# Optimization experiments

Measured on AMD Instinct MI355X. Metric: run time of the kernel, lower is better.

The kernel has to match this reference:

```python
import jax, jax.numpy as jnp
import numpy as np

B, L, LE = 2, 1024, 1024
NM, DM, NL = 80, 512, 8
LAYERS = NL // 2
DS, EXP, K, H = 16, 2, 4, 4
DI = EXP * DM            # 1024
DTR = (DM + 15) // 16    # dt_rank 'auto' -> 32
HD = DM // H             # 128


def setup_inputs() -> dict:
    key = jax.random.key(0)
    ks = iter(jax.random.split(key, 48))
    n = lambda shape, s=0.02: jax.random.normal(next(ks), shape, jnp.float32) * s
    return {
        "x": jax.random.normal(next(ks), (B, L, NM), jnp.float32),
        "enc_output": jax.random.normal(next(ks), (B, LE, DM), jnp.float32),
        "W_in": n((DM, NM)), "b_in": jnp.zeros((DM,), jnp.float32),
        "m_norm_w": jnp.ones((LAYERS, DM), jnp.float32),
        "m_in_w": n((LAYERS, 2 * DI, DM)),
        "m_conv_w": n((LAYERS, DI, K), 0.1),
        "m_conv_b": jnp.zeros((LAYERS, DI), jnp.float32),
        "m_xproj_w": n((LAYERS, DTR + 2 * DS, DI)),
        "m_dt_w": n((LAYERS, DI, DTR)),
        "m_dt_b": n((LAYERS, DI), 0.1),
        "m_Alog": jnp.tile(jnp.log(jnp.arange(1, DS + 1, dtype=jnp.float32))[None, None, :], (LAYERS, DI, 1)),
        "m_D": jnp.ones((LAYERS, DI), jnp.float32),
        "m_out_w": n((LAYERS, DM, DI)),
        "a_in_w": n((LAYERS, 3 * DM, DM)),
        "a_in_b": jnp.zeros((LAYERS, 3 * DM), jnp.float32),
        "a_out_w": n((LAYERS, DM, DM)),
        "a_out_b": jnp.zeros((LAYERS, DM), jnp.float32),
        "a_ln_w": jnp.ones((LAYERS, DM), jnp.float32),
        "a_ln_b": jnp.zeros((LAYERS, DM), jnp.float32),
        "normf_w": jnp.ones((DM,), jnp.float32),
        "W_out": n((NM, DM)),
    }


def rmsnorm(x, w, eps=1e-5):
    return x * jax.lax.rsqrt(jnp.mean(x * x, axis=-1, keepdims=True) + eps) * w


def layernorm(x, w, b, eps=1e-5):
    m = jnp.mean(x, axis=-1, keepdims=True)
    v = jnp.mean((x - m) ** 2, axis=-1, keepdims=True)
    return (x - m) * jax.lax.rsqrt(v + eps) * w + b


def dwconv_causal(x, w, b):
    # x: (B,L,DI), w: (DI,K) depthwise; torch Conv1d(padding=K-1)[..., :L] == left-pad K-1
    xt = jnp.transpose(x, (0, 2, 1))  # (B,DI,L)
    y = jax.lax.conv_general_dilated(xt, w[:, None, :], (1,), [(K - 1, 0)],
                                     feature_group_count=DI,
                                     dimension_numbers=("NCH", "OIH", "NCH"))
    return jnp.transpose(y, (0, 2, 1)) + b


def selective_scan_cumsum(u, delta, A, Bm, Cm, Dv):
    # mamba-tiny 'cumsum' scan. u,delta: (B,L,DI); A: (DI,DS); Bm,Cm: (B,L,DS); Dv: (DI,)
    dA = jnp.einsum("bld,dn->bldn", delta, A)
    dBu = jnp.einsum("bld,bld,bln->bldn", delta, u, Bm)
    shifted = jnp.pad(dA[:, 1:], ((0, 0), (0, 1), (0, 0), (0, 0)))
    dA_cs = jnp.exp(jnp.flip(jnp.cumsum(jnp.flip(shifted, 1), 1), 1))  # suffix-sum exp
    xs = jnp.cumsum(dBu * dA_cs, axis=1) / (dA_cs + 1e-12)
    y = jnp.einsum("bldn,bln->bld", xs, Cm)
    return y + u * Dv


def mamba_block(u, in_w, conv_w, conv_b, xproj_w, dt_w, dt_b, Alog, Dv, out_w):
    xr = u @ in_w.T                       # (B,L,2*DI)
    xm, res = xr[..., :DI], xr[..., DI:]
    xm = jax.nn.silu(dwconv_causal(xm, conv_w, conv_b))
    x_dbl = xm @ xproj_w.T                # (B,L,DTR+2*DS)
    dlt = x_dbl[..., :DTR]
    Bm = x_dbl[..., DTR:DTR + DS]
    Cm = x_dbl[..., DTR + DS:]
    delta = jax.nn.softplus(dlt @ dt_w.T + dt_b)
    A = -jnp.exp(Alog)
    y = selective_scan_cumsum(xm, delta, A, Bm, Cm, Dv)
    y = y * jax.nn.silu(res)
    return y @ out_w.T


def cross_attn_block(q_in, kv, in_w, in_b, out_w, out_b, ln_w, ln_b):
    Wq, Wk, Wv = in_w[:DM], in_w[DM:2 * DM], in_w[2 * DM:]
    bq, bk, bv = in_b[:DM], in_b[DM:2 * DM], in_b[2 * DM:]
    q = (q_in @ Wq.T + bq).reshape(B, -1, H, HD)
    k = (kv @ Wk.T + bk).reshape(B, -1, H, HD)
    v = (kv @ Wv.T + bv).reshape(B, -1, H, HD)
    scores = jnp.einsum("bqhd,bkhd->bhqk", q, k) / jnp.sqrt(jnp.float32(HD))
    attn = jax.nn.softmax(scores, axis=-1)
    o = jnp.einsum("bhqk,bkhd->bqhd", attn, v).reshape(B, -1, DM)
    o = o @ out_w.T + out_b
    return layernorm(q_in + o, ln_w, ln_b)  # dropout is identity in eval


def reference(x, enc_output, W_in, b_in, m_norm_w, m_in_w, m_conv_w, m_conv_b,
              m_xproj_w, m_dt_w, m_dt_b, m_Alog, m_D, m_out_w,
              a_in_w, a_in_b, a_out_w, a_out_b, a_ln_w, a_ln_b, normf_w, W_out):
    h = x @ W_in.T + b_in
    for i in range(LAYERS):
        h = h + mamba_block(rmsnorm(h, m_norm_w[i]), m_in_w[i], m_conv_w[i],
                            m_conv_b[i], m_xproj_w[i], m_dt_w[i], m_dt_b[i],
                            m_Alog[i], m_D[i], m_out_w[i])
        h = cross_attn_block(h, enc_output, a_in_w[i], a_in_b[i],
                             a_out_w[i], a_out_b[i], a_ln_w[i], a_ln_b[i])
    h = rmsnorm(h, normf_w)
    return h @ W_out.T
```

## Files before the change

### kernel.cpp

```cpp
#include <hip/hip_runtime.h>
#include <hip/hip_bf16.h>
#include <math.h>

typedef __hip_bfloat16 bf16;
typedef __attribute__((ext_vector_type(8))) short short8x;
typedef __attribute__((ext_vector_type(4))) float f32x4;

static constexpr int cB   = 2;
static constexpr int cL   = 1024;
static constexpr int cLE  = 1024;
static constexpr int cNM  = 80;
static constexpr int cDM  = 512;
static constexpr int cLAYERS = 4;
static constexpr int cDS  = 16;
static constexpr int cKC  = 4;
static constexpr int cH   = 4;
static constexpr int cDI  = 1024;
static constexpr int cDTR = 32;
static constexpr int cHD  = 128;

static constexpr int cNCH = 64;
static constexpr int cCHL = cL / cNCH;

#define GLL16(g, l) __builtin_amdgcn_global_load_lds( \
    (const __attribute__((address_space(1))) void*)(g), \
    (__attribute__((address_space(3))) void*)(l), 16, 0, 0)

template<int ACT, int BM, int BN>
__global__ __launch_bounds__(256)
void bgemm_kernel(const bf16* __restrict__ A, const bf16* __restrict__ W,
                  const float* __restrict__ bias, const float* __restrict__ addv,
                  float* __restrict__ Cf, bf16* __restrict__ Cb,
                  int M, int N, int Kd, int lda, int ldw, int ldcf, int ldcb, int ldadd,
                  int bdiv, long sA1, long sA2, long sW1, long sW2,
                  long sCf1, long sCf2, long sCb1, long sCb2, long sBias)
{
    constexpr int RM = BM / 32;
    constexpr int RN = BN / 32;
    const int z = blockIdx.z;
    const int i1 = z / bdiv, i2 = z % bdiv;
    A += i1 * sA1 + i2 * sA2;
    W += i1 * sW1 + i2 * sW2;
    if (bias) bias += i1 * sBias;

    const int bm = blockIdx.y * BM;
    const int bn = blockIdx.x * BN;
    const int tid = threadIdx.x;
    const int lane = tid & 63;
    const int wid = tid >> 6;
    const int wr = wid >> 1, wc = wid & 1;

    __shared__ bf16 As[BM * 32];
    __shared__ bf16 Bs[BN * 32];

    f32x4 acc[RM][RN] = {};

    const int r_in = lane >> 2;
    const int kb   = (lane & 3) * 8;
    const int hi   = lane >> 4;
    const int rc   = lane & 15;

    for (int k0 = 0; k0 < Kd; k0 += 32) {
#pragma unroll
        for (int iss = 0; iss < BM / 64; iss++) {
            const int row = wid * (BM / 4) + iss * 16 + r_in;
            int gm = bm + row; if (gm >= M) gm = M - 1;
            const bf16* ga = A + (long)gm * lda + k0 + kb;
            GLL16(ga, As + (wid * (BM / 4) + iss * 16) * 32);
        }
#pragma unroll
        for (int iss = 0; iss < BN / 64; iss++) {
            const int row = wid * (BN / 4) + iss * 16 + r_in;
            int gn = bn + row; if (gn >= N) gn = N - 1;
            const bf16* gb = W + (long)gn * ldw + k0 + kb;
            GLL16(gb, Bs + (wid * (BN / 4) + iss * 16) * 32);
        }
        asm volatile("s_waitcnt vmcnt(0)" ::: "memory");
        __syncthreads();

        short8x af[RM], bfv[RN];
#pragma unroll
        for (int i = 0; i < RM; i++)
            af[i] = *(const short8x*)(As + (wr * (BM / 2) + i * 16 + rc) * 32 + hi * 8);
#pragma unroll
        for (int j = 0; j < RN; j++)
            bfv[j] = *(const short8x*)(Bs + (wc * (BN / 2) + j * 16 + rc) * 32 + hi * 8);
#pragma unroll
        for (int i = 0; i < RM; i++)
#pragma unroll
            for (int j = 0; j < RN; j++)
                acc[i][j] = __builtin_amdgcn_mfma_f32_16x16x32_bf16(af[i], bfv[j], acc[i][j], 0, 0, 0);
        __syncthreads();
    }

    const long cfo = i1 * sCf1 + i2 * sCf2;
    const long cbo = i1 * sCb1 + i2 * sCb2;
#pragma unroll
    for (int i = 0; i < RM; i++) {
#pragma unroll
        for (int r = 0; r < 4; r++) {
            const int gm = bm + wr * (BM / 2) + i * 16 + hi * 4 + r;
            if (gm >= M) continue;
#pragma unroll
            for (int j = 0; j < RN; j++) {
                const int gn = bn + wc * (BN / 2) + j * 16 + rc;
                if (gn >= N) continue;
                float v = acc[i][j][r];
                if (bias) v += bias[gn];
                if (ACT == 1) v = (v > 20.f) ? v : log1pf(__expf(v));
                if (addv) v += addv[cfo + (long)gm * ldadd + gn];
                if (Cf) Cf[cfo + (long)gm * ldcf + gn] = v;
                if (Cb) Cb[cbo + (long)gm * ldcb + gn] = __float2bfloat16(v);
            }
        }
    }
}

static inline void bgemm(int ACT, int BM, int BN, const bf16* A, const bf16* W, const float* bias,
                         const float* addv, float* Cf, bf16* Cb,
                         int M, int N, int Kd, int lda, int ldw, int ldcf, int ldcb, int ldadd,
                         int nz, int bdiv, long sA1, long sA2, long sW1, long sW2,
                         long sCf1, long sCf2, long sCb1, long sCb2, long sBias, hipStream_t s)
{
    dim3 g((N + BN - 1) / BN, (M + BM - 1) / BM, nz), b(256);
#define BG_ARGS A, W, bias, addv, Cf, Cb, M, N, Kd, lda, ldw, ldcf, ldcb, ldadd, \
                bdiv, sA1, sA2, sW1, sW2, sCf1, sCf2, sCb1, sCb2, sBias
    if (BM == 128) {
        if (ACT == 1) bgemm_kernel<1, 128, 128><<<g, b, 0, s>>>(BG_ARGS);
        else          bgemm_kernel<0, 128, 128><<<g, b, 0, s>>>(BG_ARGS);
    } else if (BN == 128) {
        if (ACT == 1) bgemm_kernel<1, 64, 128><<<g, b, 0, s>>>(BG_ARGS);
        else          bgemm_kernel<0, 64, 128><<<g, b, 0, s>>>(BG_ARGS);
    } else {
        bgemm_kernel<0, 64, 64><<<g, b, 0, s>>>(BG_ARGS);
    }
#undef BG_ARGS
}

static inline void bgemm_plain(int ACT, int BM, int BN, const bf16* A, const bf16* W,
                               const float* bias, const float* addv, float* Cf, bf16* Cb,
                               int M, int N, int Kd, int lda, int ldw, int ldcf, int ldcb,
                               int ldadd, hipStream_t s)
{
    bgemm(ACT, BM, BN, A, W, bias, addv, Cf, Cb, M, N, Kd, lda, ldw, ldcf, ldcb, ldadd,
          1, 1, 0, 0, 0, 0, 0, 0, 0, 0, 0, s);
}

__global__ __launch_bounds__(128)
void flash_attn_kernel(const bf16* __restrict__ Hb, const bf16* __restrict__ Wq,
                       const float* __restrict__ bq,
                       const bf16* __restrict__ Kp, const bf16* __restrict__ VTp,
                       bf16* __restrict__ Op, float scale)
{
    const int qt = blockIdx.x;
    const int bh = blockIdx.y;
    const int b = bh >> 2, h = bh & 3;
    const int tid = threadIdx.x;
    const int w = tid >> 6;
    const int lane = tid & 63;
    const int rc = lane & 15, hi = lane >> 4;
    const int rlo = rc & 7;
    const int r_in = lane >> 2;
    const int kb   = (lane & 3) * 8;

    __shared__ bf16 Qs[32 * 128];
    __shared__ bf16 Ks[64 * 128];
    __shared__ bf16 Vs[128 * 64];
    __shared__ bf16 Ps[32 * 64];

    {
        bf16* HsT = Vs;
        bf16* WsT = Ks;
        const bf16* hb0 = Hb + ((long)(b * cL + qt * 32)) * cDM;
        const bf16* wq0 = Wq + (long)h * cHD * cDM;
        f32x4 qacc[8] = {};
        for (int k0 = 0; k0 < cDM; k0 += 32) {
            __syncthreads();
            GLL16(hb0 + (long)(w * 16 + r_in) * cDM + k0 + kb, HsT + (w * 16) * 32);
#pragma unroll
            for (int iss = 0; iss < 4; iss++)
                GLL16(wq0 + (long)(iss * 32 + w * 16 + r_in) * cDM + k0 + kb,
                      WsT + (iss * 32 + w * 16) * 32);
            asm volatile("s_waitcnt vmcnt(0)" ::: "memory");
            __syncthreads();
            short8x aH = *(const short8x*)(HsT + (w * 16 + rc) * 32 + hi * 8);
#pragma unroll
            for (int j = 0; j < 8; j++) {
                short8x bW = *(const short8x*)(WsT + (j * 16 + rc) * 32 + hi * 8);
                qacc[j] = __builtin_amdgcn_mfma_f32_16x16x32_bf16(aH, bW, qacc[j], 0, 0, 0);
            }
        }
        __syncthreads();
#pragma unroll
        for (int j2 = 0; j2 < 8; j2++)
#pragma unroll
            for (int r = 0; r < 4; r++) {
                const int qrow = w * 16 + hi * 4 + r;
                const int col = j2 * 16 + rc;
                const float qv = qacc[j2][r] + bq[h * cHD + col];
                Qs[qrow * 128 + (((col >> 3) ^ (qrow & 7)) << 3) + (col & 7)] =
                    __float2bfloat16(qv);
            }
    }
    __syncthreads();

    short8x aq[4];
#pragma unroll
    for (int kk = 0; kk < 4; kk++) {
        const int sc = (kk * 4 + hi) ^ rlo;
        aq[kk] = *(const short8x*)(Qs + (w * 16 + rc) * 128 + sc * 8);
    }

    float m_r[4], l_r[4];
#pragma unroll
    for (int r = 0; r < 4; r++) { m_r[r] = -1e30f; l_r[r] = 0.f; }
    f32x4 oacc[8] = {};

    const bf16* kb0 = Kp + ((long)(b * cLE)) * (2 * cDM) + h * cHD;
    const bf16* vb0 = VTp + ((long)(b * cDM + h * cHD)) * cLE;

    for (int kt = 0; kt < 16; kt++) {
        __syncthreads();
#pragma unroll
        for (int c = 0; c < 8; c++) {
            const int row = w * 32 + c * 4 + (lane >> 4);
            const int gc = (lane & 15) ^ (row & 7);
            GLL16(kb0 + ((long)(kt * 64 + row)) * (2 * cDM) + gc * 8,
                  Ks + (w * 32 + c * 4) * 128);
        }
#pragma unroll
        for (int c = 0; c < 8; c++) {
            const int row = w * 64 + c * 8 + (lane >> 3);
            const int gc = (lane & 7) ^ (row & 7);
            GLL16(vb0 + (long)row * cLE + kt * 64 + gc * 8,
                  Vs + (w * 64 + c * 8) * 64);
        }
        asm volatile("s_waitcnt vmcnt(0)" ::: "memory");
        __syncthreads();

        f32x4 s[4] = {};
#pragma unroll
        for (int kk = 0; kk < 4; kk++) {
            const int sc = (kk * 4 + hi) ^ rlo;
#pragma unroll
            for (int j = 0; j < 4; j++) {
                short8x bk = *(const short8x*)(Ks + (j * 16 + rc) * 128 + sc * 8);
                s[j] = __builtin_amdgcn_mfma_f32_16x16x32_bf16(aq[kk], bk, s[j], 0, 0, 0);
            }
        }

        float p[4][4];
        float esc[4];
#pragma unroll
        for (int r = 0; r < 4; r++) {
            const float v0 = s[0][r] * scale, v1 = s[1][r] * scale;
            const float v2 = s[2][r] * scale, v3 = s[3][r] * scale;
            float mx = fmaxf(fmaxf(v0, v1), fmaxf(v2, v3));
            mx = fmaxf(mx, __shfl_xor(mx, 1));
            mx = fmaxf(mx, __shfl_xor(mx, 2));
            mx = fmaxf(mx, __shfl_xor(mx, 4));
            mx = fmaxf(mx, __shfl_xor(mx, 8));
            const float mn = fmaxf(m_r[r], mx);
            p[0][r] = __expf(v0 - mn);
            p[1][r] = __expf(v1 - mn);
            p[2][r] = __expf(v2 - mn);
            p[3][r] = __expf(v3 - mn);
            float rs = (p[0][r] + p[1][r]) + (p[2][r] + p[3][r]);
            rs += __shfl_xor(rs, 1);
            rs += __shfl_xor(rs, 2);
            rs += __shfl_xor(rs, 4);
            rs += __shfl_xor(rs, 8);
            esc[r] = __expf(m_r[r] - mn);
            l_r[r] = l_r[r] * esc[r] + rs;
            m_r[r] = mn;
        }
#pragma unroll
        for (int j2 = 0; j2 < 8; j2++)
#pragma unroll
            for (int r = 0; r < 4; r++)
                oacc[j2][r] *= esc[r];
#pragma unroll
        for (int j = 0; j < 4; j++)
#pragma unroll
            for (int r = 0; r < 4; r++) {
                const int q = w * 16 + hi * 4 + r;
                const int cp = (j * 2 + (rc >> 3)) ^ (q & 7);
                Ps[q * 64 + cp * 8 + (rc & 7)] = __float2bfloat16(p[j][r]);
            }
        __syncthreads();
#pragma unroll
        for (int ks = 0; ks < 2; ks++) {
            const int sc = (ks * 4 + hi) ^ rlo;
            short8x ap = *(const short8x*)(Ps + (w * 16 + rc) * 64 + sc * 8);
#pragma unroll
            for (int j2 = 0; j2 < 8; j2++) {
                short8x bv = *(const short8x*)(Vs + (j2 * 16 + rc) * 64 + sc * 8);
                oacc[j2] = __builtin_amdgcn_mfma_f32_16x16x32_bf16(ap, bv, oacc[j2], 0, 0, 0);
            }
        }
    }

    float inv[4];
#pragma unroll
    for (int r = 0; r < 4; r++) inv[r] = 1.f / l_r[r];
    bf16* ob = Op + ((long)(b * cL + qt * 32)) * cDM + h * cHD;
#pragma unroll
    for (int j2 = 0; j2 < 8; j2++)
#pragma unroll
        for (int r = 0; r < 4; r++)
            ob[(long)(w * 16 + hi * 4 + r) * cDM + j2 * 16 + rc] =
                __float2bfloat16(oacc[j2][r] * inv[r]);
}

__global__ void splitk_reduce_kernel(const float* __restrict__ parts, float* __restrict__ outf,
                                     bf16* __restrict__ outb, int n4, int sliceN4, int S)
{
    const int i = blockIdx.x * 256 + threadIdx.x;
    if (i >= n4) return;
    float4 a = ((const float4*)parts)[i];
    for (int s2 = 1; s2 < S; s2++) {
        float4 b2 = ((const float4*)parts)[i + (long)s2 * sliceN4];
        a.x += b2.x; a.y += b2.y; a.z += b2.z; a.w += b2.w;
    }
    ((float4*)outf)[i] = a;
    bf16 b0 = __float2bfloat16(a.x), b1 = __float2bfloat16(a.y);
    bf16 b2 = __float2bfloat16(a.z), b3 = __float2bfloat16(a.w);
    short4 pk = { *(short*)&b0, *(short*)&b1, *(short*)&b2, *(short*)&b3 };
    ((short4*)outb)[i] = pk;
}

__global__ void cvt_all_kernel(
    const float* __restrict__ s0, bf16* __restrict__ d0,
    const float* __restrict__ s1, bf16* __restrict__ d1,
    const float* __restrict__ s2, bf16* __restrict__ d2,
    const float* __restrict__ s3, bf16* __restrict__ d3,
    const float* __restrict__ s4, bf16* __restrict__ d4,
    const float* __restrict__ s5, bf16* __restrict__ d5,
    const float* __restrict__ s6, bf16* __restrict__ d6,
    const float* __restrict__ s7, bf16* __restrict__ d7)
{
    constexpr long E0 = 1048576, E1 = 4194304, E2 = 262144, E3 = 131072;
    constexpr long E4 = 2097152, E5 = 3145728, E6 = 1048576, E7 = 40960;
    constexpr long C0 = E0, C1 = C0 + E1, C2 = C1 + E2, C3 = C2 + E3;
    constexpr long C4 = C3 + E4, C5 = C4 + E5, C6 = C5 + E6, C7 = C6 + E7;
    long i = ((long)blockIdx.x * 256 + threadIdx.x) * 4;
    if (i >= C7) return;
    const float* s; bf16* d;
    if      (i < C0) { s = s0; d = d0; }
    else if (i < C1) { s = s1; d = d1; i -= C0; }
    else if (i < C2) { s = s2; d = d2; i -= C1; }
    else if (i < C3) { s = s3; d = d3; i -= C2; }
    else if (i < C4) { s = s4; d = d4; i -= C3; }
    else if (i < C5) { s = s5; d = d5; i -= C4; }
    else if (i < C6) { s = s6; d = d6; i -= C5; }
    else             { s = s7; d = d7; i -= C6; }
    float4 v = *(const float4*)(s + i);
    d[i]     = __float2bfloat16(v.x);
    d[i + 1] = __float2bfloat16(v.y);
    d[i + 2] = __float2bfloat16(v.z);
    d[i + 3] = __float2bfloat16(v.w);
}

__global__ void cvt_pad_kernel(const float* __restrict__ in, bf16* __restrict__ out,
                               int rows, int kin, int kout)
{
    const int idx = blockIdx.x * 256 + threadIdx.x;
    if (idx >= rows * kout) return;
    const int r = idx / kout, k = idx - r * kout;
    out[idx] = __float2bfloat16(k < kin ? in[(long)r * kin + k] : 0.f);
}

__global__ void transpose_bf16_kernel(const bf16* __restrict__ in, bf16* __restrict__ out,
                                      int ldin, int col0, long inLS, long outLS)
{
    __shared__ bf16 t[32][33];
    const int z = blockIdx.z;
    const int lay = z >> 1, b = z & 1;
    in  += (long)lay * inLS;
    out += (long)lay * outLS;
    const int le0 = blockIdx.x * 32, d0 = blockIdx.y * 32;
    const int tid = threadIdx.x;
    const int c = tid & 31, r = tid >> 5;
    for (int i = r; i < 32; i += 8)
        t[i][c] = in[((long)b * cLE + le0 + i) * ldin + col0 + d0 + c];
    __syncthreads();
    for (int i = r; i < 32; i += 8)
        out[((long)b * cDM + d0 + i) * cLE + le0 + c] = t[c][i];
}

__global__ void rmsnorm_kernel(const float* __restrict__ x, const float* __restrict__ w,
                               float* __restrict__ outf, bf16* __restrict__ outb, int Dm)
{
    const int row = blockIdx.x;
    const float* xr = x + (long)row * Dm;
    float s = 0.f;
    for (int i = threadIdx.x; i < Dm; i += 256) { float v = xr[i]; s += v * v; }
    __shared__ float red[5];
    const int lane = threadIdx.x & 63, wv = threadIdx.x >> 6;
#pragma unroll
    for (int off = 1; off < 64; off <<= 1) s += __shfl_xor(s, off);
    if (lane == 0) red[wv] = s;
    __syncthreads();
    if (threadIdx.x == 0) {
        float t = red[0] + red[1] + red[2] + red[3];
        red[4] = rsqrtf(t / Dm + 1e-5f);
    }
    __syncthreads();
    const float scale = red[4];
    for (int i = threadIdx.x; i < Dm; i += 256) {
        float v = xr[i] * scale * w[i];
        if (outf) outf[(long)row * Dm + i] = v;
        if (outb) outb[(long)row * Dm + i] = __float2bfloat16(v);
    }
}

__global__ void layernorm_kernel(const float* __restrict__ x, const float* __restrict__ w,
                                 const float* __restrict__ b, float* __restrict__ outf,
                                 bf16* __restrict__ outb,
                                 const float* __restrict__ rms_w, bf16* __restrict__ rms_out)
{
    const int row = blockIdx.x;
    const float* xr = x + (long)row * 512;
    const int t = threadIdx.x;
    const int i0 = t, i1 = t + 256;
    float x0 = xr[i0], x1 = xr[i1];
    float s = x0 + x1, sq = x0 * x0 + x1 * x1;
    __shared__ float red[8];
    __shared__ float mv[2];
    const int lane = t & 63, wv = t >> 6;
#pragma unroll
    for (int off = 1; off < 64; off <<= 1) { s += __shfl_xor(s, off); sq += __shfl_xor(sq, off); }
    if (lane == 0) { red[wv] = s; red[4 + wv] = sq; }
    __syncthreads();
    if (t == 0) {
        float ts = red[0] + red[1] + red[2] + red[3];
        float tq = red[4] + red[5] + red[6] + red[7];
        float m = ts / 512.f;
        float var = tq / 512.f - m * m;
        mv[0] = m;
        mv[1] = rsqrtf(var + 1e-5f);
    }
    __syncthreads();
    const float m = mv[0], rs = mv[1];
    const float v0 = (x0 - m) * rs * w[i0] + b[i0];
    const float v1 = (x1 - m) * rs * w[i1] + b[i1];
    outf[(long)row * 512 + i0] = v0;
    outf[(long)row * 512 + i1] = v1;
    outb[(long)row * 512 + i0] = __float2bfloat16(v0);
    outb[(long)row * 512 + i1] = __float2bfloat16(v1);
    float s2 = v0 * v0 + v1 * v1;
#pragma unroll
    for (int off = 1; off < 64; off <<= 1) s2 += __shfl_xor(s2, off);
    if (lane == 0) red[wv] = s2;
    __syncthreads();
    if (t == 0) mv[0] = rsqrtf((red[0] + red[1] + red[2] + red[3]) / 512.f + 1e-5f);
    __syncthreads();
    const float rsc = mv[0];
    rms_out[(long)row * 512 + i0] = __float2bfloat16(v0 * rsc * rms_w[i0]);
    rms_out[(long)row * 512 + i1] = __float2bfloat16(v1 * rsc * rms_w[i1]);
}

__global__ void conv_silu_kernel(const float* __restrict__ xr, const float* __restrict__ w,
                                 const float* __restrict__ bias, float* __restrict__ xm,
                                 bf16* __restrict__ xmb)
{
    const int idx = blockIdx.x * 256 + threadIdx.x;
    if (idx >= cB * cL * cDI) return;
    const int d = idx & (cDI - 1);
    const int l = (idx >> 10) & (cL - 1);
    const int b = idx >> 20;
    float s = bias[d];
#pragma unroll
    for (int j = 0; j < cKC; j++) {
        const int ls = l + j - (cKC - 1);
        if (ls >= 0) s += w[d * cKC + j] * xr[((long)(b * cL + ls)) * (2 * cDI) + d];
    }
    s = s / (1.f + __expf(-s));
    xm[(long)idx] = s;
    xmb[(long)idx] = __float2bfloat16(s);
}

__global__ void scan_phase1(const float* __restrict__ xm, const float* __restrict__ delta,
                            const float* __restrict__ xdbl, const float* __restrict__ Alog,
                            float* __restrict__ aprod_out, float* __restrict__ send_out)
{
    const int idx4 = blockIdx.x * 256 + threadIdx.x;
    const int ng = idx4 & 3;
    const int d  = (idx4 >> 2) & (cDI - 1);
    const int ch = (idx4 >> 12) & (cNCH - 1);
    const int b  = idx4 >> 18;
    const float4 Al = *(const float4*)(Alog + d * cDS + 4 * ng);
    const float A0 = -__expf(Al.x), A1 = -__expf(Al.y), A2 = -__expf(Al.z), A3 = -__expf(Al.w);
    float s0 = 0.f, s1 = 0.f, s2 = 0.f, s3 = 0.f;
    float p0 = 1.f, p1 = 1.f, p2 = 1.f, p3 = 1.f;
    const int l0 = ch * cCHL;
    const float* dp = delta + (long)(b * cL + l0) * cDI + d;
    const float* up = xm    + (long)(b * cL + l0) * cDI + d;
    const float* xb = xdbl  + (long)(b * cL + l0) * 64 + cDTR + 4 * ng;
#pragma unroll
    for (int t = 0; t < cCHL; t++) {
        const float dl = dp[(long)t * cDI];
        const float du = dl * up[(long)t * cDI];
        const float4 Bv = *(const float4*)(xb + (long)t * 64);
        const float a0 = __expf(dl * A0), a1 = __expf(dl * A1);
        const float a2 = __expf(dl * A2), a3 = __expf(dl * A3);
        s0 = a0 * s0 + du * Bv.x; p0 *= a0;
        s1 = a1 * s1 + du * Bv.y; p1 *= a1;
        s2 = a2 * s2 + du * Bv.z; p2 *= a2;
        s3 = a3 * s3 + du * Bv.w; p3 *= a3;
    }
    const long base4 = (((long)(b * cNCH + ch) * cDI + d) * cDS) + 4 * ng;
    float4 pv = { p0, p1, p2, p3 };
    float4 sv = { s0, s1, s2, s3 };
    *(float4*)(aprod_out + base4) = pv;
    *(float4*)(send_out + base4)  = sv;
}

__global__ void scan_phase2(const float* __restrict__ aprod, const float* __restrict__ send,
                            float* __restrict__ sinit)
{
    const int j = blockIdx.x * 64 + threadIdx.x;
    const int n = j & (cDS - 1);
    const int d = (j >> 4) & (cDI - 1);
    const int b = j >> 14;
    float s = 0.f;
#pragma unroll
    for (int c = 0; c < cNCH; c++) {
        const long off = (((long)(b * cNCH + c) * cDI + d) * cDS) + n;
        sinit[off] = s;
        s = aprod[off] * s + send[off];
    }
}

__global__ void scan_phase3(const float* __restrict__ xm, const float* __restrict__ delta,
                            const float* __restrict__ xdbl, const float* __restrict__ Alog,
                            const float* __restrict__ Dv, const float* __restrict__ xr,
                            const float* __restrict__ sinit, bf16* __restrict__ y)
{
    const int idx4 = blockIdx.x * 256 + threadIdx.x;
    const int ng = idx4 & 3;
    const int d  = (idx4 >> 2) & (cDI - 1);
    const int ch = (idx4 >> 12) & (cNCH - 1);
    const int b  = idx4 >> 18;
    const float4 Al = *(const float4*)(Alog + d * cDS + 4 * ng);
    const float A0 = -__expf(Al.x), A1 = -__expf(Al.y), A2 = -__expf(Al.z), A3 = -__expf(Al.w);
    const float Dval = Dv[d];
    const long base4 = (((long)(b * cNCH + ch) * cDI + d) * cDS) + 4 * ng;
    float4 st = *(const float4*)(sinit + base4);
    float s0 = st.x, s1 = st.y, s2 = st.z, s3 = st.w;
    const int l0 = ch * cCHL;
    const float* dp = delta + (long)(b * cL + l0) * cDI + d;
    const float* up = xm    + (long)(b * cL + l0) * cDI + d;
    const float* xb = xdbl  + (long)(b * cL + l0) * 64 + cDTR + 4 * ng;
    const float* xc = xb + cDS;
    const float* rp = xr + (long)(b * cL + l0) * (2 * cDI) + cDI + d;
    bf16* yp = y + (long)(b * cL + l0) * cDI + d;
#pragma unroll
    for (int t = 0; t < cCHL; t++) {
        const float dl = dp[(long)t * cDI];
        const float u  = up[(long)t * cDI];
        const float du = dl * u;
        const float4 Bv = *(const float4*)(xb + (long)t * 64);
        const float4 Cv = *(const float4*)(xc + (long)t * 64);
        const float a0 = __expf(dl * A0), a1 = __expf(dl * A1);
        const float a2 = __expf(dl * A2), a3 = __expf(dl * A3);
        s0 = a0 * s0 + du * Bv.x;
        s1 = a1 * s1 + du * Bv.y;
        s2 = a2 * s2 + du * Bv.z;
        s3 = a3 * s3 + du * Bv.w;
        float c = s0 * Cv.x;
        c = fmaf(s1, Cv.y, c);
        c = fmaf(s2, Cv.z, c);
        c = fmaf(s3, Cv.w, c);
        c += __shfl_xor(c, 1);
        c += __shfl_xor(c, 2);
        if (ng == 0) {
            const float res = rp[(long)t * 2 * cDI];
            const float sig = 1.f / (1.f + __expf(-res));
            yp[(long)t * cDI] = __float2bfloat16((c + u * Dval) * (res * sig));
        }
    }
}

extern "C" void kernel_launch(void* const* d_in, const int* in_sizes, int n_in,
                              void* d_out, int out_size, void* d_ws, size_t ws_size,
                              hipStream_t stream)
{
    const float* x       = (const float*)d_in[0];
    const float* enc     = (const float*)d_in[1];
    const float* W_in    = (const float*)d_in[2];
    const float* b_in    = (const float*)d_in[3];
    const float* m_norm_w= (const float*)d_in[4];
    const float* m_in_w  = (const float*)d_in[5];
    const float* m_conv_w= (const float*)d_in[6];
    const float* m_conv_b= (const float*)d_in[7];
    const float* m_xproj = (const float*)d_in[8];
    const float* m_dt_w  = (const float*)d_in[9];
    const float* m_dt_b  = (const float*)d_in[10];
    const float* m_Alog  = (const float*)d_in[11];
    const float* m_D     = (const float*)d_in[12];
    const float* m_out_w = (const float*)d_in[13];
    const float* a_in_w  = (const float*)d_in[14];
    const float* a_in_b  = (const float*)d_in[15];
    const float* a_out_w = (const float*)d_in[16];
    const float* a_out_b = (const float*)d_in[17];
    const float* a_ln_w  = (const float*)d_in[18];
    const float* a_ln_b  = (const float*)d_in[19];
    const float* normf_w = (const float*)d_in[20];
    const float* W_out   = (const float*)d_in[21];
    float* out = (float*)d_out;

    float* ws = (float*)d_ws;
    long off = 0;
    auto allocf = [&](long n) { float* p = ws + off; off += n; return p; };

    const long M1 = 1 << 20;
    float* bufH    = allocf(M1);
    float* bufPre  = allocf(M1);
    float* bufXR   = allocf(4 * M1);
    float* bufXM   = allocf(2 * M1);
    float* bufDelta= allocf(2 * M1);
    float* bufXDBL = allocf(M1 / 8);
    bf16* bufU    = (bf16*)allocf(M1 / 2);
    bf16* bufHb   = (bf16*)allocf(M1 / 2);
    bf16* bufXMb  = (bf16*)allocf(M1);
    bf16* bufXDBLb= (bf16*)allocf(M1 / 16);
    bf16* bufY    = (bf16*)allocf(M1);
    bf16* bufO    = (bf16*)allocf(M1 / 2);
    bf16* encb    = (bf16*)allocf(M1 / 2);
    bf16* w_in_b  = (bf16*)allocf(2 * M1);
    bf16* w_xp_b  = (bf16*)allocf(M1 / 8);
    bf16* w_dt_b  = (bf16*)allocf(M1 / 16);
    bf16* w_out_b = (bf16*)allocf(M1);
    bf16* w_ain_b = (bf16*)allocf(3 * M1 / 2);
    bf16* w_aout_b= (bf16*)allocf(M1 / 2);
    bf16* x_pad   = (bf16*)allocf(2048L * 96 / 2);
    bf16* w_inp_b = (bf16*)allocf(512L * 96 / 2);
    bf16* w_outf_b= (bf16*)allocf(80L * 512 / 2);
    float* bufAP  = allocf(2 * M1);
    float* bufSE  = allocf(2 * M1);
    float* bufSI  = allocf(2 * M1);
    bf16* bufKV4  = (bf16*)allocf(4 * M1);
    bf16* bufVT4  = (bf16*)allocf(2 * M1);

    const int Mrows = cB * cL;
    const long SUMSZ4 = (long)cB * cNCH * cDI * 4;
    const long kvLS = (long)Mrows * 2 * cDM;
    const long vtLS = (long)cB * cDM * cLE;

    cvt_all_kernel<<<11688, 256, 0, stream>>>(
        enc, encb, m_in_w, w_in_b, m_xproj, w_xp_b, m_dt_w, w_dt_b,
        m_out_w, w_out_b, a_in_w, w_ain_b, a_out_w, w_aout_b, W_out, w_outf_b);
    cvt_pad_kernel<<<(Mrows * 96 + 255) / 256, 256, 0, stream>>>(x, x_pad, Mrows, cNM, 96);
    cvt_pad_kernel<<<(cDM * 96 + 255) / 256, 256, 0, stream>>>(W_in, w_inp_b, cDM, cNM, 96);

    bgemm(0, 64, 128, encb, w_ain_b + (long)cDM * cDM, a_in_b + cDM, nullptr, nullptr, bufKV4,
          Mrows, 2 * cDM, cDM, cDM, cDM, 0, 2 * cDM, 0,
          cLAYERS, 1,
          0, 0,
          (long)3 * cDM * cDM, 0,
          0, 0, kvLS, 0,
          (long)3 * cDM,
          stream);
    {
        dim3 g(cLE / 32, cDM / 32, cLAYERS * cB);
        transpose_bf16_kernel<<<g, 256, 0, stream>>>(bufKV4, bufVT4, 2 * cDM, cDM, kvLS, vtLS);
    }

    bgemm_plain(0, 64, 64, x_pad, w_inp_b, b_in, nullptr, bufH, nullptr,
                Mrows, cDM, 96, 96, 96, cDM, 0, 0, stream);
    rmsnorm_kernel<<<Mrows, 256, 0, stream>>>(bufH, m_norm_w, nullptr, bufU, cDM);

    for (int i = 0; i < cLAYERS; i++) {
        const bf16*  in_w   = w_in_b   + (long)i * 2 * cDI * cDM;
        const float* conv_w = m_conv_w + (long)i * cDI * cKC;
        const float* conv_b = m_conv_b + (long)i * cDI;
        const bf16*  xproj  = w_xp_b   + (long)i * 64 * cDI;
        const bf16*  dt_w   = w_dt_b   + (long)i * cDI * cDTR;
        const float* dt_b   = m_dt_b   + (long)i * cDI;
        const float* Alog   = m_Alog   + (long)i * cDI * cDS;
        const float* Dv     = m_D      + (long)i * cDI;
        const bf16*  out_w  = w_out_b  + (long)i * cDM * cDI;
        const bf16*  ain_w  = w_ain_b  + (long)i * 3 * cDM * cDM;
        const float* ain_b  = a_in_b   + (long)i * 3 * cDM;
        const bf16*  aout_w = w_aout_b + (long)i * cDM * cDM;
        const float* aout_b = a_out_b  + (long)i * cDM;
        const float* ln_w   = a_ln_w   + (long)i * cDM;
        const float* ln_b   = a_ln_b   + (long)i * cDM;
        const bf16*  kv_l   = bufKV4 + (long)i * kvLS;
        const bf16*  vt_l   = bufVT4 + (long)i * vtLS;
        const float* next_rms_w = (i + 1 < cLAYERS) ? (m_norm_w + (long)(i + 1) * cDM) : normf_w;

        bgemm_plain(0, 64, 128, bufU, in_w, nullptr, nullptr, bufXR, nullptr,
                    Mrows, 2 * cDI, cDM, cDM, cDM, 2 * cDI, 0, 0, stream);
        conv_silu_kernel<<<(cB * cL * cDI) / 256, 256, 0, stream>>>(bufXR, conv_w, conv_b, bufXM, bufXMb);
        bgemm(0, 64, 64, bufXMb, xproj, nullptr, nullptr, bufPre, nullptr,
              Mrows, 64, cDI / 8, cDI, cDI, 64, 0, 0,
              8, 1, 128, 0, 128, 0, (long)Mrows * 64, 0, 0, 0, 0, stream);
        splitk_reduce_kernel<<<(Mrows * 64 / 4 + 255) / 256, 256, 0, stream>>>(
            bufPre, bufXDBL, bufXDBLb, Mrows * 64 / 4, Mrows * 64 / 4, 8);
        bgemm_plain(1, 64, 128, bufXDBLb, dt_w, dt_b, nullptr, bufDelta, nullptr,
                    Mrows, cDI, cDTR, 64, cDTR, cDI, 0, 0, stream);
        scan_phase1<<<(int)(SUMSZ4 / 256), 256, 0, stream>>>(bufXM, bufDelta, bufXDBL, Alog, bufAP, bufSE);
        scan_phase2<<<(cB * cDI * cDS) / 64, 64, 0, stream>>>(bufAP, bufSE, bufSI);
        scan_phase3<<<(int)(SUMSZ4 / 256), 256, 0, stream>>>(bufXM, bufDelta, bufXDBL, Alog, Dv, bufXR, bufSI, bufY);
        bgemm_plain(0, 64, 64, bufY, out_w, nullptr, bufH, bufH, bufHb,
                    Mrows, cDM, cDI, cDI, cDI, cDM, cDM, cDM, stream);

        {
            dim3 g(cL / 32, cB * cH);
            flash_attn_kernel<<<g, 128, 0, stream>>>(bufHb, ain_w, ain_b, kv_l, vt_l, bufO,
                                                     0.08838834764831845f);
        }
        bgemm_plain(0, 64, 64, bufO, aout_w, aout_b, bufH, bufPre, nullptr,
                    Mrows, cDM, cDM, cDM, cDM, cDM, 0, cDM, stream);
        layernorm_kernel<<<Mrows, 256, 0, stream>>>(bufPre, ln_w, ln_b, bufH, bufHb,
                                                    next_rms_w, bufU);
    }

    bgemm_plain(0, 64, 64, bufU, w_outf_b, nullptr, nullptr, out, nullptr,
                Mrows, cNM, cDM, cDM, cDM, cNM, 0, 0, stream);
}
```

Baseline: 770.3 us.

## Split flash attention over key blocks and move Q projection to a GEMM

The fused Q-projection inside the attention kernel is replaced by a separate bf16 GEMM that writes Q. The attention kernel is split along the key dimension into four chunks, giving four times as many blocks (256 to 1024), and writes unnormalized fp32 partial outputs plus per-row max and sum. A new combine kernel merges the partials with log-sum-exp weights. This targets low occupancy on a GPU with many compute units, at the cost of two extra launches and extra fp32 partial traffic.

```diff
diff --git a/kernel.cpp b/kernel.cpp
--- a/kernel.cpp
+++ b/kernel.cpp
@@ -21,6 +21,7 @@
 
 static constexpr int cNCH = 64;
 static constexpr int cCHL = cL / cNCH;
+static constexpr int cSPL = 4;
 
 #define GLL16(g, l) __builtin_amdgcn_global_load_lds( \
     (const __attribute__((address_space(1))) void*)(g), \
@@ -147,69 +148,42 @@
 }
 
 __global__ __launch_bounds__(128)
-void flash_attn_kernel(const bf16* __restrict__ Hb, const bf16* __restrict__ Wq,
-                       const float* __restrict__ bq,
-                       const bf16* __restrict__ Kp, const bf16* __restrict__ VTp,
-                       bf16* __restrict__ Op, float scale)
+void flash_split_kernel(const bf16* __restrict__ Qp, const bf16* __restrict__ Kp,
+                        const bf16* __restrict__ VTp, float* __restrict__ OP,
+                        float2* __restrict__ ML, float scale)
 {
     const int qt = blockIdx.x;
     const int bh = blockIdx.y;
+    const int sp = blockIdx.z;
     const int b = bh >> 2, h = bh & 3;
     const int tid = threadIdx.x;
     const int w = tid >> 6;
     const int lane = tid & 63;
     const int rc = lane & 15, hi = lane >> 4;
     const int rlo = rc & 7;
-    const int r_in = lane >> 2;
-    const int kb   = (lane & 3) * 8;
-
-    __shared__ bf16 Qs[32 * 128];
+
     __shared__ bf16 Ks[64 * 128];
     __shared__ bf16 Vs[128 * 64];
     __shared__ bf16 Ps[32 * 64];
 
     {
-        bf16* HsT = Vs;
-        bf16* WsT = Ks;
-        const bf16* hb0 = Hb + ((long)(b * cL + qt * 32)) * cDM;
-        const bf16* wq0 = Wq + (long)h * cHD * cDM;
-        f32x4 qacc[8] = {};
-        for (int k0 = 0; k0 < cDM; k0 += 32) {
-            __syncthreads();
-            GLL16(hb0 + (long)(w * 16 + r_in) * cDM + k0 + kb, HsT + (w * 16) * 32);
-#pragma unroll
-            for (int iss = 0; iss < 4; iss++)
-                GLL16(wq0 + (long)(iss * 32 + w * 16 + r_in) * cDM + k0 + kb,
-                      WsT + (iss * 32 + w * 16) * 32);
-            asm volatile("s_waitcnt vmcnt(0)" ::: "memory");
-            __syncthreads();
-            short8x aH = *(const short8x*)(HsT + (w * 16 + rc) * 32 + hi * 8);
-#pragma unroll
-            for (int j = 0; j < 8; j++) {
-                short8x bW = *(const short8x*)(WsT + (j * 16 + rc) * 32 + hi * 8);
-                qacc[j] = __builtin_amdgcn_mfma_f32_16x16x32_bf16(aH, bW, qacc[j], 0, 0, 0);
-            }
-        }
-        __syncthreads();
-#pragma unroll
-        for (int j2 = 0; j2 < 8; j2++)
-#pragma unroll
-            for (int r = 0; r < 4; r++) {
-                const int qrow = w * 16 + hi * 4 + r;
-                const int col = j2 * 16 + rc;
-                const float qv = qacc[j2][r] + bq[h * cHD + col];
-                Qs[qrow * 128 + (((col >> 3) ^ (qrow & 7)) << 3) + (col & 7)] =
-                    __float2bfloat16(qv);
-            }
-    }
-    __syncthreads();
-
+        const bf16* qb = Qp + ((long)(b * cL + qt * 32)) * cDM + h * cHD;
+#pragma unroll
+        for (int c = 0; c < 4; c++) {
+            const int row = w * 16 + c * 4 + (lane >> 4);
+            const int gc = (lane & 15) ^ (row & 7);
+            GLL16(qb + (long)row * cDM + gc * 8, Ks + (w * 16 + c * 4) * 128);
+        }
+    }
+    asm volatile("s_waitcnt vmcnt(0)" ::: "memory");
+    __syncthreads();
     short8x aq[4];
 #pragma unroll
     for (int kk = 0; kk < 4; kk++) {
         const int sc = (kk * 4 + hi) ^ rlo;
-        aq[kk] = *(const short8x*)(Qs + (w * 16 + rc) * 128 + sc * 8);
-    }
+        aq[kk] = *(const short8x*)(Ks + (w * 16 + rc) * 128 + sc * 8);
+    }
+    __syncthreads();
 
     float m_r[4], l_r[4];
 #pragma unroll
@@ -219,7 +193,8 @@
     const bf16* kb0 = Kp + ((long)(b * cLE)) * (2 * cDM) + h * cHD;
     const bf16* vb0 = VTp + ((long)(b * cDM + h * cHD)) * cLE;
 
-    for (int kt = 0; kt < 16; kt++) {
+    for (int t = 0; t < 4; t++) {
+        const int kt = sp * 4 + t;
         __syncthreads();
 #pragma unroll
         for (int c = 0; c < 8; c++) {
@@ -300,16 +275,59 @@
         }
     }
 
-    float inv[4];
-#pragma unroll
-    for (int r = 0; r < 4; r++) inv[r] = 1.f / l_r[r];
-    bf16* ob = Op + ((long)(b * cL + qt * 32)) * cDM + h * cHD;
+    float* ob = OP + (((long)sp * (cB * cL) + b * cL + qt * 32)) * cDM + h * cHD;
 #pragma unroll
     for (int j2 = 0; j2 < 8; j2++)
 #pragma unroll
         for (int r = 0; r < 4; r++)
-            ob[(long)(w * 16 + hi * 4 + r) * cDM + j2 * 16 + rc] =
-                __float2bfloat16(oacc[j2][r] * inv[r]);
+            ob[(long)(w * 16 + hi * 4 + r) * cDM + j2 * 16 + rc] = oacc[j2][r];
+    if (rc == 0) {
+#pragma unroll
+        for (int r = 0; r < 4; r++) {
+            const int row = qt * 32 + w * 16 + hi * 4 + r;
+            ML[(((long)sp * cB + b) * cH + h) * cL + row] = make_float2(m_r[r], l_r[r]);
+        }
+    }
+}
+
+__global__ __launch_bounds__(256)
+void flash_combine_kernel(const float* __restrict__ OP, const float2* __restrict__ ML,
+                          bf16* __restrict__ Op)
+{
+    const int row = blockIdx.x;
+    const int b = row >> 10, lr = row & 1023;
+    const int t = threadIdx.x;
+    __shared__ float ms[cSPL][cH], ls[cSPL][cH];
+    __shared__ float wgt[cSPL][cH], linv[cH];
+    if (t < cSPL * cH) {
+        const int s = t >> 2, h = t & 3;
+        float2 v = ML[(((long)s * cB + b) * cH + h) * cL + lr];
+        ms[s][h] = v.x; ls[s][h] = v.y;
+    }
+    __syncthreads();
+    if (t < cH) {
+        const int h = t;
+        float M = fmaxf(fmaxf(ms[0][h], ms[1][h]), fmaxf(ms[2][h], ms[3][h]));
+        float L = 0.f;
+#pragma unroll
+        for (int s = 0; s < cSPL; s++) {
+            const float e = __expf(ms[s][h] - M);
+            wgt[s][h] = e;
+            L += e * ls[s][h];
+        }
+        linv[h] = 1.f / L;
+    }
+    __syncthreads();
+#pragma unroll
+    for (int c0 = 0; c0 < 2; c0++) {
+        const int col = t + c0 * 256;
+        const int h = col >> 7;
+        float o = 0.f;
+#pragma unroll
+        for (int s = 0; s < cSPL; s++)
+            o += wgt[s][h] * OP[((long)s * (cB * cL) + row) * cDM + col];
+        Op[(long)row * cDM + col] = __float2bfloat16(o * linv[h]);
+    }
 }
 
 __global__ void splitk_reduce_kernel(const float* __restrict__ parts, float* __restrict__ outf,
@@ -626,6 +644,7 @@
     bf16* bufXMb  = (bf16*)allocf(M1);
     bf16* bufXDBLb= (bf16*)allocf(M1 / 16);
     bf16* bufY    = (bf16*)allocf(M1);
+    bf16* bufQ    = (bf16*)allocf(M1 / 2);
     bf16* bufO    = (bf16*)allocf(M1 / 2);
     bf16* encb    = (bf16*)allocf(M1 / 2);
     bf16* w_in_b  = (bf16*)allocf(2 * M1);
@@ -642,6 +661,8 @@
     float* bufSI  = allocf(2 * M1);
     bf16* bufKV4  = (bf16*)allocf(4 * M1);
     bf16* bufVT4  = (bf16*)allocf(2 * M1);
+    float* bufOP  = allocf(4 * M1);
+    float2* bufML = (float2*)allocf(M1 / 16);
 
     const int Mrows = cB * cL;
     const long SUMSZ4 = (long)cB * cNCH * cDI * 4;
@@ -707,11 +728,14 @@
         bgemm_plain(0, 64, 64, bufY, out_w, nullptr, bufH, bufH, bufHb,
                     Mrows, cDM, cDI, cDI, cDI, cDM, cDM, cDM, stream);
 
+        bgemm_plain(0, 64, 64, bufHb, ain_w, ain_b, nullptr, nullptr, bufQ,
+                    Mrows, cDM, cDM, cDM, cDM, 0, cDM, 0, stream);
         {
-            dim3 g(cL / 32, cB * cH);
-            flash_attn_kernel<<<g, 128, 0, stream>>>(bufHb, ain_w, ain_b, kv_l, vt_l, bufO,
-                                                     0.08838834764831845f);
-        }
+            dim3 g(cL / 32, cB * cH, cSPL);
+            flash_split_kernel<<<g, 128, 0, stream>>>(bufQ, kv_l, vt_l, bufOP, bufML,
+                                                      0.08838834764831845f);
+        }
+        flash_combine_kernel<<<Mrows, 256, 0, stream>>>(bufOP, bufML, bufO);
         bgemm_plain(0, 64, 64, bufO, aout_w, aout_b, bufH, bufPre, nullptr,
                     Mrows, cDM, cDM, cDM, cDM, cDM, 0, cDM, stream);
         layernorm_kernel<<<Mrows, 256, 0, stream>>>(bufPre, ln_w, ln_b, bufH, bufHb,
```

After: 741.1 us, median of 2. -3.8%, faster.
